# Performance work log

Hardware: AMD Instinct MI355X
Metric: run time of the kernel (lower is better)

The kernel has to match this reference:

```python
import jax, jax.numpy as jnp
import numpy as np

GROUPS = 32  # from analyze_enhance_linear_ops(4096, 4096, 0.05): smallest divisor g with 1/g <= 0.05


def setup_inputs() -> dict:
    key = jax.random.key(0)
    k1, k2, k3, k4, k5 = jax.random.split(key, 5)
    B, S, D_in, D_out = 4, 2048, 4096, 4096
    ig = D_out // GROUPS  # 128
    x = jax.random.normal(k1, (B, S, D_in), dtype=jnp.float32)
    W = jax.random.normal(k2, (D_out, D_in), dtype=jnp.float32) * 0.02
    b = jax.random.normal(k3, (D_out,), dtype=jnp.float32) * 0.02
    Wg = jax.random.normal(k4, (GROUPS, ig, ig), dtype=jnp.float32) * 0.02
    bg = jax.random.normal(k5, (GROUPS, ig), dtype=jnp.float32) * 0.02
    return {"x": x, "W": W, "b": b, "Wg": Wg, "bg": bg}


def reference(x, W, b, Wg, bg):
    # original_linear: dense GEMM, torch Linear layout W[out, in]
    y = jnp.einsum('bsi,oi->bso', x, W) + b            # [B, S, D_out]
    # GroupedLinear: block-diagonal transform over groups of size out_group
    B, S, D = y.shape
    G, og, ig = Wg.shape
    yg = y.reshape(B, S, G, ig)                        # split into groups
    out = jnp.einsum('bsgi,goi->bsgo', yg, Wg) + bg    # per-group small GEMM + bias
    return out.reshape(B, S, D)                        # cat along feature dim
```

## Files before the change

kernel.cpp:

```cpp
#include <hip/hip_runtime.h>
#include <hip/hip_bf16.h>
#include <stdint.h>

typedef float f32x4 __attribute__((ext_vector_type(4)));
typedef short s16x8 __attribute__((ext_vector_type(8)));
typedef unsigned int u32x2 __attribute__((ext_vector_type(2)));
typedef unsigned int u32x4 __attribute__((ext_vector_type(4)));

#define MDIM 8192
#define NDIM 4096
#define KDIM 4096
#define NKT  64

__device__ __forceinline__ unsigned pkbf(float lo, float hi) {
  unsigned short l = __builtin_bit_cast(unsigned short, __float2bfloat16(lo));
  unsigned short h = __builtin_bit_cast(unsigned short, __float2bfloat16(hi));
  return ((unsigned)h << 16) | (unsigned)l;
}

__device__ __forceinline__ void gload16(const void* g, void* l) {
  __builtin_amdgcn_global_load_lds((const __attribute__((address_space(1))) int*)g,
                                   (__attribute__((address_space(3))) int*)l, 16, 0, 0);
}

__global__ __launch_bounds__(256) void conv_tile(
    const float* __restrict__ X, const float* __restrict__ W,
    s16x8* __restrict__ wsA, s16x8* __restrict__ wsB) {
  __shared__ char lds[32768];
  const int b = blockIdx.x;
  const int tid = threadIdx.x;
  const float* src;
  s16x8* dst;
  int bi;
  if (b < 32 * NKT) { src = X; dst = wsA; bi = b; }
  else              { src = W; dst = wsB; bi = b - 32 * NKT; }
  const int rt = bi >> 6;
  const int kt = bi & 63;
  const int fr = tid >> 4;
  const int c4 = (tid & 15) * 4;
  const int h = c4 >> 5, q = (c4 >> 3) & 3, eh = (c4 >> 2) & 1;
  #pragma unroll
  for (int f = 0; f < 16; ++f) {
    const int row = f * 16 + fr;
    f32x4 v = *(const f32x4*)(src + ((size_t)rt * 256 + row) * KDIM + kt * 64 + c4);
    u32x2 p = { pkbf(v[0], v[1]), pkbf(v[2], v[3]) };
    *(u32x2*)(lds + (h * 16 + f) * 1024 + (q * 16 + fr) * 16 + eh * 8) = p;
  }
  __syncthreads();
  const size_t ob = (size_t)bi * 2048;
  #pragma unroll
  for (int i = 0; i < 8; ++i)
    dst[ob + i * 256 + tid] = *(const s16x8*)(lds + (i * 256 + tid) * 16);
}

__global__ __launch_bounds__(512, 2) void gemm256(
    const s16x8* __restrict__ wsA, const s16x8* __restrict__ wsB,
    const float* __restrict__ bias, const float* __restrict__ Wg,
    const float* __restrict__ bg, float* __restrict__ out) {
  extern __shared__ char smem[];
  const int tid = threadIdx.x;
  const int lane = tid & 63;
  const int wid = tid >> 6;
  const int wr = wid >> 2;
  const int wc = wid & 3;
  const int fr = lane & 15;
  const int q4 = lane >> 4;

  const int bid = blockIdx.x;
  const int swz = (bid & 7) * 64 + (bid >> 3);
  const int bm = swz >> 4;
  const int bn = swz & 15;

  const size_t aBase = (size_t)bm * NKT * 2048;
  const size_t bBase = (size_t)bn * NKT * 2048;

  auto stage = [&](int kt, int db, int isB, int h) {
    const s16x8* s = (isB ? wsB + bBase : wsA + aBase)
                     + (size_t)kt * 2048 + h * 1024 + wid * 128 + lane;
    char* d = smem + isB * 65536 + db * 32768 + h * 16384 + wid * 2048;
    gload16(s, d);
    gload16(s + 64, d + 1024);
  };

  const char* aRd = smem + wr * 8192 + lane * 16;
  const char* bRd = smem + 65536 + wc * 4096 + lane * 16;

  f32x4 acc[8][4];
  #pragma unroll
  for (int m = 0; m < 8; ++m)
    #pragma unroll
    for (int n = 0; n < 4; ++n) acc[m][n] = (f32x4)0.0f;

  s16x8 af[4], bfr[4];

#define PHASE(DB, H, MH, SKT, SDB, SOP, SH, DOVM)                              \
  {                                                                            \
    stage(SKT, SDB, SOP, SH);                                                  \
    if ((MH) == 0) {                                                           \
      _Pragma("unroll")                                                        \
      for (int n = 0; n < 4; ++n)                                              \
        bfr[n] = *(const s16x8*)(bRd + (DB)*32768 + (H)*16384 + n * 1024);     \
    }                                                                          \
    _Pragma("unroll")                                                          \
    for (int m = 0; m < 4; ++m)                                                \
      af[m] = *(const s16x8*)(aRd + (DB)*32768 + (H)*16384 + ((MH)*4 + m) * 1024); \
    if (DOVM) asm volatile("s_waitcnt vmcnt(6)" ::: "memory");                 \
    __builtin_amdgcn_s_barrier();                                              \
    asm volatile("s_waitcnt lgkmcnt(0)" ::: "memory");                         \
    __builtin_amdgcn_s_setprio(1);                                             \
    _Pragma("unroll")                                                          \
    for (int m = 0; m < 4; ++m) {                                              \
      _Pragma("unroll")                                                        \
      for (int n = 0; n < 4; ++n)                                              \
        acc[(MH)*4 + m][n] = __builtin_amdgcn_mfma_f32_16x16x32_bf16(          \
            af[m], bfr[n], acc[(MH)*4 + m][n], 0, 0, 0);                       \
    }                                                                          \
    __builtin_amdgcn_s_setprio(0);                                             \
    __builtin_amdgcn_s_barrier();                                              \
  }

  stage(0, 0, 0, 0); stage(0, 0, 1, 0); stage(0, 0, 0, 1); stage(0, 0, 1, 1);
  stage(1, 1, 0, 0); stage(1, 1, 1, 0); stage(1, 1, 1, 1);
  asm volatile("s_waitcnt vmcnt(3)" ::: "memory");
  __builtin_amdgcn_s_barrier();

  for (int it = 0; it < 32; ++it) {
    const int u0 = 2 * it;
    const int k1 = u0 + 1;
    const int k2 = (u0 + 2 < NKT) ? u0 + 2 : NKT - 1;
    const int k3 = (u0 + 3 < NKT) ? u0 + 3 : NKT - 1;
    PHASE(0, 0, 0, k1, 1, 0, 1, 0)
    PHASE(0, 0, 1, k2, 0, 1, 0, 0)
    PHASE(0, 1, 0, k2, 0, 0, 0, 0)
    PHASE(0, 1, 1, k2, 0, 1, 1, 1)
    PHASE(1, 0, 0, k2, 0, 0, 1, 0)
    PHASE(1, 0, 1, k3, 1, 1, 0, 0)
    PHASE(1, 1, 0, k3, 1, 0, 0, 0)
    PHASE(1, 1, 1, k3, 1, 1, 1, 1)
  }
#undef PHASE

  asm volatile("s_waitcnt vmcnt(0)" ::: "memory");
  __builtin_amdgcn_s_barrier();

  float bv[4];
  #pragma unroll
  for (int n = 0; n < 4; ++n) bv[n] = bias[bn * 256 + wc * 64 + n * 16 + fr];

  #pragma unroll
  for (int m = 0; m < 8; ++m) {
    const int Mf = wr * 8 + m;
    #pragma unroll
    for (int np = 0; np < 2; ++np) {
      const int Kh = wc * 2 + np;
      #pragma unroll
      for (int j = 0; j < 8; ++j) {
        const int nn = np * 2 + (j >> 2);
        const int r = (j + q4) & 3;
        const int qq = (j >> 2) * 2 + (fr >> 3);
        const int frs = q4 * 4 + r;
        const float y = acc[m][nn][r] + bv[nn];
        *(unsigned short*)(smem + (Mf * 8 + Kh) * 1024 + (qq * 16 + frs) * 16 + (fr & 7) * 2)
            = __builtin_bit_cast(unsigned short, __float2bfloat16(y));
      }
    }
  }
  asm volatile("s_waitcnt lgkmcnt(0)" ::: "memory");
  __builtin_amdgcn_s_barrier();

  const int g = bn * 2 + (wc >> 1);
  const float* wgb = Wg + (size_t)g * 16384;
  f32x4 acc2[8][4];
  #pragma unroll
  for (int m = 0; m < 8; ++m)
    #pragma unroll
    for (int n = 0; n < 4; ++n) acc2[m][n] = (f32x4)0.0f;

  #pragma unroll
  for (int s = 0; s < 4; ++s) {
    const int Kh = (wc >> 1) * 4 + s;
    s16x8 af2[8];
    #pragma unroll
    for (int m = 0; m < 8; ++m)
      af2[m] = *(const s16x8*)(smem + ((wr * 8 + m) * 8 + Kh) * 1024 + lane * 16);
    #pragma unroll
    for (int n = 0; n < 4; ++n) {
      const int ocl = (wc & 1) * 64 + n * 16 + fr;
      const float* wp = wgb + ocl * 128 + s * 32 + q4 * 8;
      f32x4 w0 = *(const f32x4*)wp;
      f32x4 w1 = *(const f32x4*)(wp + 4);
      u32x4 pw = { pkbf(w0[0], w0[1]), pkbf(w0[2], w0[3]),
                   pkbf(w1[0], w1[1]), pkbf(w1[2], w1[3]) };
      const s16x8 bfw = __builtin_bit_cast(s16x8, pw);
      #pragma unroll
      for (int m = 0; m < 8; ++m)
        acc2[m][n] = __builtin_amdgcn_mfma_f32_16x16x32_bf16(af2[m], bfw, acc2[m][n], 0, 0, 0);
    }
  }

  float bgv[4];
  #pragma unroll
  for (int n = 0; n < 4; ++n) bgv[n] = bg[bn * 256 + wc * 64 + n * 16 + fr];

  #pragma unroll
  for (int m = 0; m < 8; ++m) {
    #pragma unroll
    for (int n = 0; n < 4; ++n) {
      const int col = bn * 256 + wc * 64 + n * 16 + fr;
      #pragma unroll
      for (int r = 0; r < 4; ++r) {
        const size_t row = (size_t)bm * 256 + wr * 128 + m * 16 + q4 * 4 + r;
        out[row * NDIM + col] = acc2[m][n][r] + bgv[n];
      }
    }
  }
}

extern "C" void kernel_launch(void* const* d_in, const int* in_sizes, int n_in,
                              void* d_out, int out_size, void* d_ws, size_t ws_size,
                              hipStream_t stream) {
  const float* X    = (const float*)d_in[0];
  const float* W    = (const float*)d_in[1];
  const float* bias = (const float*)d_in[2];
  const float* Wg   = (const float*)d_in[3];
  const float* bg   = (const float*)d_in[4];
  float* out = (float*)d_out;

  s16x8* wsA = (s16x8*)d_ws;
  s16x8* wsB = wsA + ((size_t)MDIM * KDIM / 8);

  hipFuncSetAttribute(reinterpret_cast<const void*>(gemm256),
                      hipFuncAttributeMaxDynamicSharedMemorySize, 131072);

  conv_tile<<<dim3(3072), dim3(256), 0, stream>>>(X, W, wsA, wsB);
  gemm256<<<dim3(512), dim3(512), 131072, stream>>>(wsA, wsB, bias, Wg, bg, out);
}
```

Measured before the change: 298.2 us.

## Double-buffer LDS fragment registers to prefetch next phase during MFMA

Splits the A and B fragment registers into ping-pong pairs so that each phase issues the LDS reads for the next phase's fragments before running MFMAs on the current ones. The wait drops from lgkmcnt(0) to lgkmcnt(4) or lgkmcnt(8), and sched_barriers pin the ordering. The aim is to hide LDS read latency behind matrix math instead of stalling at each barrier. In exchange it needs more VGPRs for the fragments and has to reason carefully that the prefetch reads land after the matching global-to-LDS stage has completed.

```diff
diff --git a/kernel.cpp b/kernel.cpp
--- a/kernel.cpp
+++ b/kernel.cpp
@@ -91,29 +91,51 @@
     #pragma unroll
     for (int n = 0; n < 4; ++n) acc[m][n] = (f32x4)0.0f;
 
-  s16x8 af[4], bfr[4];
-
-#define PHASE(DB, H, MH, SKT, SDB, SOP, SH, DOVM)                              \
+  s16x8 afA[4], afB[4], bfrX[4], bfrY[4];
+
+#define PHASE_R4(MH, AFC, BFC, AFN, RDB, RH, RMH, SKT, SDB, SOP, SH)           \
   {                                                                            \
     stage(SKT, SDB, SOP, SH);                                                  \
-    if ((MH) == 0) {                                                           \
-      _Pragma("unroll")                                                        \
-      for (int n = 0; n < 4; ++n)                                              \
-        bfr[n] = *(const s16x8*)(bRd + (DB)*32768 + (H)*16384 + n * 1024);     \
-    }                                                                          \
     _Pragma("unroll")                                                          \
     for (int m = 0; m < 4; ++m)                                                \
-      af[m] = *(const s16x8*)(aRd + (DB)*32768 + (H)*16384 + ((MH)*4 + m) * 1024); \
-    if (DOVM) asm volatile("s_waitcnt vmcnt(6)" ::: "memory");                 \
-    __builtin_amdgcn_s_barrier();                                              \
-    asm volatile("s_waitcnt lgkmcnt(0)" ::: "memory");                         \
+      AFN[m] = *(const s16x8*)(aRd + (RDB)*32768 + (RH)*16384 + ((RMH)*4 + m) * 1024); \
+    __builtin_amdgcn_sched_barrier(0);                                         \
+    __builtin_amdgcn_s_barrier();                                              \
+    asm volatile("s_waitcnt lgkmcnt(4)" ::: "memory");                         \
+    __builtin_amdgcn_sched_barrier(0);                                         \
     __builtin_amdgcn_s_setprio(1);                                             \
     _Pragma("unroll")                                                          \
     for (int m = 0; m < 4; ++m) {                                              \
       _Pragma("unroll")                                                        \
       for (int n = 0; n < 4; ++n)                                              \
         acc[(MH)*4 + m][n] = __builtin_amdgcn_mfma_f32_16x16x32_bf16(          \
-            af[m], bfr[n], acc[(MH)*4 + m][n], 0, 0, 0);                       \
+            AFC[m], BFC[n], acc[(MH)*4 + m][n], 0, 0, 0);                      \
+    }                                                                          \
+    __builtin_amdgcn_s_setprio(0);                                             \
+    __builtin_amdgcn_s_barrier();                                              \
+  }
+
+#define PHASE_R8(MH, AFC, BFC, AFN, BFN, RDB, RH, SKT, SDB, SOP, SH, DOVM)     \
+  {                                                                            \
+    stage(SKT, SDB, SOP, SH);                                                  \
+    if (DOVM) asm volatile("s_waitcnt vmcnt(6)" ::: "memory");                 \
+    _Pragma("unroll")                                                          \
+    for (int m = 0; m < 4; ++m)                                                \
+      AFN[m] = *(const s16x8*)(aRd + (RDB)*32768 + (RH)*16384 + m * 1024);     \
+    _Pragma("unroll")                                                          \
+    for (int n = 0; n < 4; ++n)                                                \
+      BFN[n] = *(const s16x8*)(bRd + (RDB)*32768 + (RH)*16384 + n * 1024);     \
+    __builtin_amdgcn_sched_barrier(0);                                         \
+    __builtin_amdgcn_s_barrier();                                              \
+    asm volatile("s_waitcnt lgkmcnt(8)" ::: "memory");                         \
+    __builtin_amdgcn_sched_barrier(0);                                         \
+    __builtin_amdgcn_s_setprio(1);                                             \
+    _Pragma("unroll")                                                          \
+    for (int m = 0; m < 4; ++m) {                                              \
+      _Pragma("unroll")                                                        \
+      for (int n = 0; n < 4; ++n)                                              \
+        acc[(MH)*4 + m][n] = __builtin_amdgcn_mfma_f32_16x16x32_bf16(          \
+            AFC[m], BFC[n], acc[(MH)*4 + m][n], 0, 0, 0);                      \
     }                                                                          \
     __builtin_amdgcn_s_setprio(0);                                             \
     __builtin_amdgcn_s_barrier();                                              \
@@ -123,24 +145,30 @@
   stage(1, 1, 0, 0); stage(1, 1, 1, 0); stage(1, 1, 1, 1);
   asm volatile("s_waitcnt vmcnt(3)" ::: "memory");
   __builtin_amdgcn_s_barrier();
+  #pragma unroll
+  for (int m = 0; m < 4; ++m) afA[m] = *(const s16x8*)(aRd + m * 1024);
+  #pragma unroll
+  for (int n = 0; n < 4; ++n) bfrX[n] = *(const s16x8*)(bRd + n * 1024);
 
   for (int it = 0; it < 32; ++it) {
     const int u0 = 2 * it;
     const int k1 = u0 + 1;
     const int k2 = (u0 + 2 < NKT) ? u0 + 2 : NKT - 1;
     const int k3 = (u0 + 3 < NKT) ? u0 + 3 : NKT - 1;
-    PHASE(0, 0, 0, k1, 1, 0, 1, 0)
-    PHASE(0, 0, 1, k2, 0, 1, 0, 0)
-    PHASE(0, 1, 0, k2, 0, 0, 0, 0)
-    PHASE(0, 1, 1, k2, 0, 1, 1, 1)
-    PHASE(1, 0, 0, k2, 0, 0, 1, 0)
-    PHASE(1, 0, 1, k3, 1, 1, 0, 0)
-    PHASE(1, 1, 0, k3, 1, 0, 0, 0)
-    PHASE(1, 1, 1, k3, 1, 1, 1, 1)
-  }
-#undef PHASE
+    PHASE_R4(0, afA, bfrX, afB, 0, 0, 1, k1, 1, 0, 1)
+    PHASE_R8(1, afB, bfrX, afA, bfrY, 0, 1, k2, 0, 1, 0, 0)
+    PHASE_R4(0, afA, bfrY, afB, 0, 1, 1, k2, 0, 0, 0)
+    PHASE_R8(1, afB, bfrY, afA, bfrX, 1, 0, k2, 0, 1, 1, 1)
+    PHASE_R4(0, afA, bfrX, afB, 1, 0, 1, k2, 0, 0, 1)
+    PHASE_R8(1, afB, bfrX, afA, bfrY, 1, 1, k3, 1, 1, 0, 0)
+    PHASE_R4(0, afA, bfrY, afB, 1, 1, 1, k3, 1, 0, 0)
+    PHASE_R8(1, afB, bfrY, afA, bfrX, 0, 0, k3, 1, 1, 1, 1)
+  }
+#undef PHASE_R4
+#undef PHASE_R8
 
   asm volatile("s_waitcnt vmcnt(0)" ::: "memory");
+  asm volatile("s_waitcnt lgkmcnt(0)" ::: "memory");
   __builtin_amdgcn_s_barrier();
 
   float bv[4];
```

Measured after the change: 298.3 us. About the same (+0.0%).

## Merge GEMM main-loop phases into four super-phases with split LDS waits

Applied to the files above, without the earlier changes.

Restructures the software-pipelined main loop so each step stages both A and B halves together and loads all eight A fragments, replacing eight phases with four. The first four-row MFMA block starts after a partial lgkmcnt wait, so the remaining LDS reads overlap with compute. Barriers per tile drop by half. The cost is higher register pressure from eight A fragments and a changed vmcnt/prefetch accounting, and it disables unrolling of the outer loop.

```diff
diff --git a/kernel.cpp b/kernel.cpp
--- a/kernel.cpp
+++ b/kernel.cpp
@@ -91,56 +91,62 @@
     #pragma unroll
     for (int n = 0; n < 4; ++n) acc[m][n] = (f32x4)0.0f;
 
-  s16x8 af[4], bfr[4];
-
-#define PHASE(DB, H, MH, SKT, SDB, SOP, SH, DOVM)                              \
+  s16x8 af[8], bfr[4];
+
+#define SP(DB, H, SKT, SDB, SH)                                                \
   {                                                                            \
-    stage(SKT, SDB, SOP, SH);                                                  \
-    if ((MH) == 0) {                                                           \
-      _Pragma("unroll")                                                        \
-      for (int n = 0; n < 4; ++n)                                              \
-        bfr[n] = *(const s16x8*)(bRd + (DB)*32768 + (H)*16384 + n * 1024);     \
-    }                                                                          \
-    _Pragma("unroll")                                                          \
-    for (int m = 0; m < 4; ++m)                                                \
-      af[m] = *(const s16x8*)(aRd + (DB)*32768 + (H)*16384 + ((MH)*4 + m) * 1024); \
-    if (DOVM) asm volatile("s_waitcnt vmcnt(6)" ::: "memory");                 \
+    stage(SKT, SDB, 0, SH);                                                    \
+    stage(SKT, SDB, 1, SH);                                                    \
+    _Pragma("unroll")                                                          \
+    for (int n = 0; n < 4; ++n)                                                \
+      bfr[n] = *(const s16x8*)(bRd + (DB)*32768 + (H)*16384 + n * 1024);       \
+    _Pragma("unroll")                                                          \
+    for (int m = 0; m < 8; ++m)                                                \
+      af[m] = *(const s16x8*)(aRd + (DB)*32768 + (H)*16384 + m * 1024);        \
+    asm volatile("s_waitcnt vmcnt(8)" ::: "memory");                           \
     __builtin_amdgcn_s_barrier();                                              \
-    asm volatile("s_waitcnt lgkmcnt(0)" ::: "memory");                         \
+    asm volatile("s_waitcnt lgkmcnt(4)" ::: "memory");                         \
     __builtin_amdgcn_s_setprio(1);                                             \
     _Pragma("unroll")                                                          \
     for (int m = 0; m < 4; ++m) {                                              \
       _Pragma("unroll")                                                        \
       for (int n = 0; n < 4; ++n)                                              \
-        acc[(MH)*4 + m][n] = __builtin_amdgcn_mfma_f32_16x16x32_bf16(          \
-            af[m], bfr[n], acc[(MH)*4 + m][n], 0, 0, 0);                       \
+        acc[m][n] = __builtin_amdgcn_mfma_f32_16x16x32_bf16(                   \
+            af[m], bfr[n], acc[m][n], 0, 0, 0);                                \
+    }                                                                          \
+    asm volatile("s_waitcnt lgkmcnt(0)" ::: "memory");                         \
+    _Pragma("unroll")                                                          \
+    for (int m = 4; m < 8; ++m) {                                              \
+      _Pragma("unroll")                                                        \
+      for (int n = 0; n < 4; ++n)                                              \
+        acc[m][n] = __builtin_amdgcn_mfma_f32_16x16x32_bf16(                   \
+            af[m], bfr[n], acc[m][n], 0, 0, 0);                                \
     }                                                                          \
     __builtin_amdgcn_s_setprio(0);                                             \
     __builtin_amdgcn_s_barrier();                                              \
   }
 
-  stage(0, 0, 0, 0); stage(0, 0, 1, 0); stage(0, 0, 0, 1); stage(0, 0, 1, 1);
-  stage(1, 1, 0, 0); stage(1, 1, 1, 0); stage(1, 1, 1, 1);
-  asm volatile("s_waitcnt vmcnt(3)" ::: "memory");
+  stage(0, 0, 0, 0); stage(0, 0, 1, 0);
+  stage(0, 0, 0, 1); stage(0, 0, 1, 1);
+  stage(1, 1, 0, 0); stage(1, 1, 1, 0);
+  asm volatile("s_waitcnt vmcnt(8)" ::: "memory");
   __builtin_amdgcn_s_barrier();
 
+  #pragma clang loop unroll(disable)
   for (int it = 0; it < 32; ++it) {
     const int u0 = 2 * it;
     const int k1 = u0 + 1;
     const int k2 = (u0 + 2 < NKT) ? u0 + 2 : NKT - 1;
     const int k3 = (u0 + 3 < NKT) ? u0 + 3 : NKT - 1;
-    PHASE(0, 0, 0, k1, 1, 0, 1, 0)
-    PHASE(0, 0, 1, k2, 0, 1, 0, 0)
-    PHASE(0, 1, 0, k2, 0, 0, 0, 0)
-    PHASE(0, 1, 1, k2, 0, 1, 1, 1)
-    PHASE(1, 0, 0, k2, 0, 0, 1, 0)
-    PHASE(1, 0, 1, k3, 1, 1, 0, 0)
-    PHASE(1, 1, 0, k3, 1, 0, 0, 0)
-    PHASE(1, 1, 1, k3, 1, 1, 1, 1)
-  }
-#undef PHASE
+    SP(0, 0, k1, 1, 1)
+    SP(0, 1, k2, 0, 0)
+    SP(1, 0, k2, 0, 1)
+    SP(1, 1, k3, 1, 0)
+  }
+#undef SP
 
   asm volatile("s_waitcnt vmcnt(0)" ::: "memory");
+  asm volatile("s_waitcnt lgkmcnt(0)" ::: "memory");
   __builtin_amdgcn_s_barrier();
 
   float bv[4];
```

Result: no change. 301.8 us (+1.2%).
